# Performance work log

Hardware: AMD Instinct MI355X
Metric: run time of the kernel (lower is better)

## Reference

```python
import jax, jax.numpy as jnp
import numpy as np

D_MODEL = 1024
NUM_HEADS = 16
HEAD_DIM = D_MODEL // NUM_HEADS  # 64
N = 1024
B = 8


def setup_inputs() -> dict:
    key = jax.random.key(0)
    ks = jax.random.split(key, 11)
    s = 0.02
    inp = {
        'query': jax.random.normal(ks[0], (B, D_MODEL, N), jnp.float32),
        'key':   jax.random.normal(ks[1], (B, D_MODEL, N), jnp.float32),
        'value': jax.random.normal(ks[2], (B, D_MODEL, N), jnp.float32),
        # 1x1 conv1d == linear over channel dim: weight [out, in], bias [out]
        'Wq': jax.random.normal(ks[3], (D_MODEL, D_MODEL), jnp.float32) * s,
        'bq': jax.random.normal(ks[4], (D_MODEL,), jnp.float32) * s,
        'Wk': jax.random.normal(ks[5], (D_MODEL, D_MODEL), jnp.float32) * s,
        'bk': jax.random.normal(ks[6], (D_MODEL,), jnp.float32) * s,
        'Wv': jax.random.normal(ks[7], (D_MODEL, D_MODEL), jnp.float32) * s,
        'bv': jax.random.normal(ks[8], (D_MODEL,), jnp.float32) * s,
        'Wm': jax.random.normal(ks[9], (D_MODEL, D_MODEL), jnp.float32) * s,
        'bm': jax.random.normal(ks[10], (D_MODEL,), jnp.float32) * s,
    }
    return inp


def _proj(W, b, x):
    # nn.Conv1d(kernel_size=1): out[b,o,n] = sum_i W[o,i] x[b,i,n] + b[o]
    return jnp.einsum('oi,bin->bon', W, x) + b[None, :, None]


def reference(query, key, value, Wq, bq, Wk, bk, Wv, bv, Wm, bm):
    Bd = query.shape[0]
    # view(B, dim, heads, N): channel axis split as (head_dim, num_heads)
    q = _proj(Wq, bq, query).reshape(Bd, HEAD_DIM, NUM_HEADS, -1)
    k = _proj(Wk, bk, key).reshape(Bd, HEAD_DIM, NUM_HEADS, -1)
    v = _proj(Wv, bv, value).reshape(Bd, HEAD_DIM, NUM_HEADS, -1)
    scale = 1.0 / (HEAD_DIM ** 0.5)
    scores = jnp.einsum('bdhn,bdhm->bhnm', q, k) * scale  # [B,H,N,N]
    prob = jax.nn.softmax(scores, axis=-1)
    x = jnp.einsum('bhnm,bdhm->bdhn', prob, v)  # [B,D,H,N]
    out = _proj(Wm, bm, x.reshape(Bd, HEAD_DIM * NUM_HEADS, -1))
    return out
```

## Files before the change

kernel.cpp:

```cpp
#include <hip/hip_runtime.h>

typedef __bf16 bf16x8 __attribute__((ext_vector_type(8)));
typedef __bf16 bf16x4 __attribute__((ext_vector_type(4)));
typedef float f32x4 __attribute__((ext_vector_type(4)));
typedef unsigned short u16;
typedef unsigned int u32;

typedef union { bf16x8 v8; bf16x4 v4[2]; } bfu;

__device__ __forceinline__ u16 f2bf(float f) {
  u32 u = __builtin_bit_cast(u32, f);
  u = (u + 0x7FFFu + ((u >> 16) & 1u)) >> 16;
  return (u16)u;
}

__device__ __forceinline__ void gload_lds16(const void* g, void* l) {
  __builtin_amdgcn_global_load_lds((const __attribute__((address_space(1))) void*)g,
                                   (__attribute__((address_space(3))) void*)l, 16, 0, 0);
}

__global__ __launch_bounds__(256) void transpose_cast3(const float* __restrict__ q,
                                                       const float* __restrict__ k,
                                                       const float* __restrict__ v,
                                                       u16* __restrict__ X3) {
  __shared__ float T[64][68];
  int tid = threadIdx.x;
  int n0 = blockIdx.x * 64, i0 = blockIdx.y * 64;
  int z = blockIdx.z;
  int which = z >> 3, b = z & 7;
  const float* src = (which == 0) ? q : (which == 1) ? k : v;
  size_t boff = (size_t)b << 20;
  const float* s = src + boff;
  u16* d = X3 + ((size_t)which << 23) + boff;
  int ir = tid >> 4, n4 = (tid & 15) * 4;
#pragma unroll
  for (int r = 0; r < 4; ++r) {
    int i_loc = ir + r * 16;
    float4 vv = *(const float4*)(s + (size_t)(i0 + i_loc) * 1024 + n0 + n4);
    *(float4*)&T[i_loc][n4] = vv;
  }
  __syncthreads();
  int nr = tid >> 3, i8 = (tid & 7) * 8;
#pragma unroll
  for (int r = 0; r < 2; ++r) {
    int n_loc = nr + r * 32;
    u32 pk[4];
#pragma unroll
    for (int j = 0; j < 4; ++j) {
      float f0 = T[i8 + 2 * j][n_loc];
      float f1 = T[i8 + 2 * j + 1][n_loc];
      pk[j] = (u32)f2bf(f0) | ((u32)f2bf(f1) << 16);
    }
    *(uint4*)(d + (size_t)(n0 + n_loc) * 1024 + i0 + i8) = make_uint4(pk[0], pk[1], pk[2], pk[3]);
  }
}

__global__ __launch_bounds__(256) void transpose_cast(const float* __restrict__ src,
                                                      u16* __restrict__ dst) {
  __shared__ float T[64][68];
  int tid = threadIdx.x;
  int n0 = blockIdx.x * 64, i0 = blockIdx.y * 64;
  size_t boff = (size_t)blockIdx.z << 20;
  const float* s = src + boff;
  u16* d = dst + boff;
  int ir = tid >> 4, n4 = (tid & 15) * 4;
#pragma unroll
  for (int r = 0; r < 4; ++r) {
    int i_loc = ir + r * 16;
    float4 v = *(const float4*)(s + (size_t)(i0 + i_loc) * 1024 + n0 + n4);
    *(float4*)&T[i_loc][n4] = v;
  }
  __syncthreads();
  int nr = tid >> 3, i8 = (tid & 7) * 8;
#pragma unroll
  for (int r = 0; r < 2; ++r) {
    int n_loc = nr + r * 32;
    u32 pk[4];
#pragma unroll
    for (int j = 0; j < 4; ++j) {
      float f0 = T[i8 + 2 * j][n_loc];
      float f1 = T[i8 + 2 * j + 1][n_loc];
      pk[j] = (u32)f2bf(f0) | ((u32)f2bf(f1) << 16);
    }
    *(uint4*)(d + (size_t)(n0 + n_loc) * 1024 + i0 + i8) = make_uint4(pk[0], pk[1], pk[2], pk[3]);
  }
}

__global__ __launch_bounds__(256) void cast_weights(const float* __restrict__ Wq,
                                                    const float* __restrict__ Wk,
                                                    const float* __restrict__ Wv,
                                                    const float* __restrict__ Wm,
                                                    u16* __restrict__ out) {
  int w = blockIdx.y;
  const float* src = (w == 0) ? Wq : (w == 1) ? Wk : (w == 2) ? Wv : Wm;
  u16* dst = out + ((size_t)w << 20);
  int o = blockIdx.x;
  int c4 = threadIdx.x * 4;
  float f[4];
  if (w < 3) {
    float4 v = *(const float4*)(src + (size_t)o * 1024 + c4);
    f[0] = v.x; f[1] = v.y; f[2] = v.z; f[3] = v.w;
  } else {
#pragma unroll
    for (int j = 0; j < 4; ++j) {
      int cp = c4 + j;
      f[j] = src[(size_t)o * 1024 + (cp & 63) * 16 + (cp >> 6)];
    }
  }
  u32 p0 = (u32)f2bf(f[0]) | ((u32)f2bf(f[1]) << 16);
  u32 p1 = (u32)f2bf(f[2]) | ((u32)f2bf(f[3]) << 16);
  *(uint2*)(dst + (size_t)o * 1024 + c4) = make_uint2(p0, p1);
}

__device__ __forceinline__ void gemm_body(const u16* __restrict__ A,
                                          const u16* __restrict__ B,
                                          const float* __restrict__ bias,
                                          void* __restrict__ Out, float escale,
                                          int epi, u16* LD) {
  int tid = threadIdx.x;
  int wave = tid >> 6, l = tid & 63, ln = l & 15, g = l >> 4;
  int wm = wave >> 1, wn = wave & 1;
  int bid = blockIdx.x;
  int mt = (bid >> 3) & 7;
  int nt = ((bid & 7) << 2) | (bid >> 6);
  int c0 = mt * 128, n0 = nt * 256;

  int R = tid >> 3;
  int v = (tid & 7) ^ (R & 7);
  const u16* aS = A + (size_t)(c0 + 2 * R + (v >> 2)) * 1024 + (v & 3) * 8;
  const u16* bS = B + (size_t)(n0 + 2 * R + (v >> 2)) * 1024 + (v & 3) * 8;

  int slr = ((((ln & 1) << 2) | g) ^ ((ln >> 1) & 7)) * 8;
  int laneA = (wm * 32 + (ln >> 1)) * 64 + slr;
  int laneB = (wn * 64 + (ln >> 1)) * 64 + slr;

  f32x4 acc[4][8] = {};

#define STAGE(buf, kt)                                                        \
  do {                                                                        \
    gload_lds16(aS + (kt) * 32, &LD[(buf) * 4096 + tid * 8]);                 \
    gload_lds16(aS + 65536 + (kt) * 32, &LD[(buf) * 4096 + 2048 + tid * 8]);  \
    gload_lds16(bS + (kt) * 32, &LD[12288 + (buf) * 8192 + tid * 8]);         \
    gload_lds16(bS + 65536 + (kt) * 32,                                       \
                &LD[12288 + (buf) * 8192 + 2048 + tid * 8]);                  \
    gload_lds16(bS + 131072 + (kt) * 32,                                      \
                &LD[12288 + (buf) * 8192 + 4096 + tid * 8]);                  \
    gload_lds16(bS + 196608 + (kt) * 32,                                      \
                &LD[12288 + (buf) * 8192 + 6144 + tid * 8]);                  \
  } while (0)

  STAGE(0, 0);
  STAGE(1, 1);

#pragma unroll
  for (int t = 0; t < 32; ++t) {
    if (t < 31)
      asm volatile("s_waitcnt vmcnt(6)" ::: "memory");
    else
      asm volatile("s_waitcnt vmcnt(0)" ::: "memory");
    asm volatile("s_barrier" ::: "memory");
    if (t <= 29) STAGE((t + 2) % 3, t + 2);
    const int ab = (t % 3) * 4096;
    const int bb = 12288 + (t % 3) * 8192;
    bf16x8 af[4];
#pragma unroll
    for (int mm = 0; mm < 4; ++mm) af[mm] = *(const bf16x8*)&LD[ab + laneA + mm * 512];
    __builtin_amdgcn_s_setprio(1);
#pragma unroll
    for (int nn = 0; nn < 8; ++nn) {
      bf16x8 bfr = *(const bf16x8*)&LD[bb + laneB + nn * 512];
#pragma unroll
      for (int mm = 0; mm < 4; ++mm)
        acc[mm][nn] = __builtin_amdgcn_mfma_f32_16x16x32_bf16(af[mm], bfr, acc[mm][nn], 0, 0, 0);
    }
    __builtin_amdgcn_s_setprio(0);
  }
#undef STAGE

  int D0 = (c0 >> 4) + wm * 4;
#pragma unroll
  for (int nn = 0; nn < 8; ++nn) {
    size_t ng = (size_t)n0 + wn * 128 + nn * 16 + ln;
#pragma unroll
    for (int r = 0; r < 4; ++r) {
      int h = g * 4 + r;
      if (epi == 0) {
        bf16x4 pk;
#pragma unroll
        for (int mm = 0; mm < 4; ++mm) {
          int c = c0 + wm * 64 + mm * 16 + h;
          pk[mm] = (__bf16)((acc[mm][nn][r] + bias[c]) * escale);
        }
        *(bf16x4*)((u16*)Out + ng * 1024 + (size_t)h * 64 + D0) = pk;
      } else {
        size_t b = ng >> 10, n = ng & 1023;
#pragma unroll
        for (int mm = 0; mm < 4; ++mm) {
          int c = c0 + wm * 64 + mm * 16 + h;
          float val = (acc[mm][nn][r] + bias[c]) * escale;
          if (epi == 1) {
            int d = D0 + mm;
            ((u16*)Out)[((b * 16 + h) * 64 + d) * 1024 + n] = f2bf(val);
          } else {
            ((float*)Out)[(b << 20) + (size_t)c * 1024 + n] = val;
          }
        }
      }
    }
  }
}

template <int EPI>
__global__ __launch_bounds__(256, 2) void gemm4b(const u16* __restrict__ A,
                                                 const u16* __restrict__ B,
                                                 const float* __restrict__ bias,
                                                 void* __restrict__ Out, float escale) {
  __shared__ u16 LD[36864];
  gemm_body(A, B, bias, Out, escale, EPI, LD);
}

__global__ __launch_bounds__(256, 2) void gemm_qkv(const u16* __restrict__ Wbf,
                                                   const u16* __restrict__ X3,
                                                   const float* __restrict__ bq,
                                                   const float* __restrict__ bk,
                                                   const float* __restrict__ bv,
                                                   u16* __restrict__ Qh,
                                                   u16* __restrict__ Kh,
                                                   u16* __restrict__ Vt, float qscale) {
  __shared__ u16 LD[36864];
  int z = blockIdx.y;
  const u16* A = Wbf + ((size_t)z << 20);
  const u16* B = X3 + ((size_t)z << 23);
  const float* bias = (z == 0) ? bq : (z == 1) ? bk : bv;
  void* Out = (z == 0) ? (void*)Qh : (z == 1) ? (void*)Kh : (void*)Vt;
  float escale = (z == 0) ? qscale : 1.0f;
  int epi = (z == 2) ? 1 : 0;
  gemm_body(A, B, bias, Out, escale, epi, LD);
}

__global__ __launch_bounds__(256, 2) void attn_kernel(const u16* __restrict__ Qh,
                                                      const u16* __restrict__ Kh,
                                                      const u16* __restrict__ Vt,
                                                      u16* __restrict__ Xh) {
  __shared__ u16 Ks[2][4096];
  __shared__ u16 Vs[2][4096];
  int tid = threadIdx.x;
  int w = tid >> 6, l = tid & 63, ln = l & 15, g = l >> 4;
  int id = blockIdx.x;
  int bh7 = id & 7;
  int qp = (id >> 3) & 3;
  int bh = (id >> 5) * 8 + bh7;
  size_t b = bh >> 4;
  int h = bh & 15;
  const u16* Qg = Qh + (b << 20) + (h << 6);
  const u16* Kg = Kh + (b << 20) + (h << 6);
  const u16* Vg = Vt + ((size_t)bh << 16);
  u16* Og = Xh + (b << 20) + (h << 6);

  bf16x8 qf[4][2];
#pragma unroll
  for (int t = 0; t < 4; ++t)
#pragma unroll
    for (int kk = 0; kk < 2; ++kk)
      qf[t][kk] = *(const bf16x8*)(Qg + (size_t)(qp * 256 + t * 64 + w * 16 + ln) * 1024 + kk * 32 + g * 8);

  int lr = l >> 3;
  int sw8 = ((l & 7) ^ lr) << 3;
  int r0 = w * 16 + lr, r1 = r0 + 8;
  const u16* kS0 = Kg + (size_t)r0 * 1024 + sw8;
  const u16* kS1 = Kg + (size_t)r1 * 1024 + sw8;
  const u16* vS0 = Vg + (size_t)r0 * 1024 + sw8;
  const u16* vS1 = Vg + (size_t)r1 * 1024 + sw8;

  f32x4 xacc[4][4] = {};
  float lacc[4] = {0.f, 0.f, 0.f, 0.f};

  gload_lds16(kS0, &Ks[0][(w * 2) * 512]);
  gload_lds16(kS1, &Ks[0][(w * 2 + 1) * 512]);
  gload_lds16(vS0, &Vs[0][(w * 2) * 512]);
  gload_lds16(vS1, &Vs[0][(w * 2 + 1) * 512]);
  __syncthreads();

  int sx = ln & 7;
  int cur = 0;
  for (int kt = 0; kt < 16; ++kt) {
    if (kt < 15) {
      int nxt = cur ^ 1;
      gload_lds16(kS0 + (size_t)(kt + 1) * 65536, &Ks[nxt][(w * 2) * 512]);
      gload_lds16(kS1 + (size_t)(kt + 1) * 65536, &Ks[nxt][(w * 2 + 1) * 512]);
      gload_lds16(vS0 + (kt + 1) * 64, &Vs[nxt][(w * 2) * 512]);
      gload_lds16(vS1 + (kt + 1) * 64, &Vs[nxt][(w * 2 + 1) * 512]);
    }
    bf16x8 kf[2][4];
#pragma unroll
    for (int kk = 0; kk < 2; ++kk)
#pragma unroll
      for (int f = 0; f < 4; ++f) {
        int slot = (((kk << 2) + g) ^ sx) << 3;
        kf[kk][f] = *(const bf16x8*)&Ks[cur][(f * 16 + ln) * 64 + slot];
      }
    bf16x8 vf[2][4];
#pragma unroll
    for (int kk = 0; kk < 2; ++kk) {
      int s0 = (kk << 2) + (g >> 1);
      int off = (g & 1) << 2;
#pragma unroll
      for (int fd = 0; fd < 4; ++fd) {
        int rowb = (fd * 16 + ln) * 64;
        bfu uv;
        uv.v4[0] = *(const bf16x4*)&Vs[cur][rowb + ((s0 ^ sx) << 3) + off];
        uv.v4[1] = *(const bf16x4*)&Vs[cur][rowb + (((s0 + 2) ^ sx) << 3) + off];
        vf[kk][fd] = uv.v8;
      }
    }
#pragma unroll
    for (int t = 0; t < 4; ++t) {
      f32x4 sacc[4] = {};
#pragma unroll
      for (int kk = 0; kk < 2; ++kk)
#pragma unroll
        for (int f = 0; f < 4; ++f)
          sacc[f] = __builtin_amdgcn_mfma_f32_16x16x32_bf16(kf[kk][f], qf[t][kk], sacc[f], 0, 0, 0);
      bf16x8 pf[2];
#pragma unroll
      for (int kk = 0; kk < 2; ++kk) {
        bfu up;
#pragma unroll
        for (int e2 = 0; e2 < 2; ++e2) {
          int f = 2 * kk + e2;
          float p0 = __builtin_amdgcn_exp2f(sacc[f][0]);
          float p1 = __builtin_amdgcn_exp2f(sacc[f][1]);
          float p2 = __builtin_amdgcn_exp2f(sacc[f][2]);
          float p3 = __builtin_amdgcn_exp2f(sacc[f][3]);
          lacc[t] += (p0 + p1) + (p2 + p3);
          bf16x4 pb;
          pb[0] = (__bf16)p0; pb[1] = (__bf16)p1; pb[2] = (__bf16)p2; pb[3] = (__bf16)p3;
          up.v4[e2] = pb;
        }
        pf[kk] = up.v8;
      }
#pragma unroll
      for (int kk = 0; kk < 2; ++kk)
#pragma unroll
        for (int fd = 0; fd < 4; ++fd)
          xacc[t][fd] = __builtin_amdgcn_mfma_f32_16x16x32_bf16(pf[kk], vf[kk][fd], xacc[t][fd], 0, 0, 0);
    }
    __syncthreads();
    cur ^= 1;
  }

#pragma unroll
  for (int t = 0; t < 4; ++t) {
    float lt = lacc[t];
    lt += __shfl_xor(lt, 16);
    lt += __shfl_xor(lt, 32);
    float il[4];
#pragma unroll
    for (int r = 0; r < 4; ++r) il[r] = 1.0f / __shfl(lt, g * 4 + r);
#pragma unroll
    for (int fd = 0; fd < 4; ++fd)
#pragma unroll
      for (int r = 0; r < 4; ++r) {
        int nq = qp * 256 + t * 64 + w * 16 + g * 4 + r;
        Og[(size_t)nq * 1024 + fd * 16 + ln] = f2bf(xacc[t][fd][r] * il[r]);
      }
  }
}

extern "C" void kernel_launch(void* const* d_in, const int* in_sizes, int n_in,
                              void* d_out, int out_size, void* d_ws, size_t ws_size,
                              hipStream_t stream) {
  const float* q  = (const float*)d_in[0];
  const float* k  = (const float*)d_in[1];
  const float* v  = (const float*)d_in[2];
  const float* Wq = (const float*)d_in[3];
  const float* bq = (const float*)d_in[4];
  const float* Wk = (const float*)d_in[5];
  const float* bk = (const float*)d_in[6];
  const float* Wv = (const float*)d_in[7];
  const float* bv = (const float*)d_in[8];
  const float* Wm = (const float*)d_in[9];
  const float* bm = (const float*)d_in[10];

  char* ws = (char*)d_ws;
  u16* Wbf = (u16*)ws;
  u16* Qh  = (u16*)(ws + (8ull << 20));
  u16* Kh  = (u16*)(ws + (24ull << 20));
  u16* Vt  = (u16*)(ws + (40ull << 20));
  u16* X3  = (u16*)(ws + (56ull << 20));

  cast_weights<<<dim3(1024, 4, 1), 256, 0, stream>>>(Wq, Wk, Wv, Wm, Wbf);

  const float qscale = 0.125f * 1.44269504088896340736f;

  if (ws_size >= (104ull << 20)) {
    transpose_cast3<<<dim3(16, 16, 24), 256, 0, stream>>>(q, k, v, X3);
    gemm_qkv<<<dim3(256, 3), 256, 0, stream>>>(Wbf, X3, bq, bk, bv, Qh, Kh, Vt, qscale);
  } else {
    dim3 tg(16, 16, 8);
    transpose_cast<<<tg, 256, 0, stream>>>(q, X3);
    gemm4b<0><<<256, 256, 0, stream>>>(Wbf, X3, bq, Qh, qscale);
    transpose_cast<<<tg, 256, 0, stream>>>(k, X3);
    gemm4b<0><<<256, 256, 0, stream>>>(Wbf + (1u << 20), X3, bk, Kh, 1.0f);
    transpose_cast<<<tg, 256, 0, stream>>>(v, X3);
    gemm4b<1><<<256, 256, 0, stream>>>(Wbf + (2u << 20), X3, bv, Vt, 1.0f);
  }

  attn_kernel<<<512, 256, 0, stream>>>(Qh, Kh, Vt, X3);

  gemm4b<2><<<256, 256, 0, stream>>>(Wbf + (3u << 20), X3, bm, d_out, 1.0f);
}
```

Before: 171.9 us.

## Rewrite QKV projection GEMM with 256x256 tiles and 8-wave blocks

Replaces the shared gemm_body call in the fused QKV projection with a dedicated kernel that uses 512 threads (8 waves in a 2x4 grid) and 256x256 output tiles. It double-buffers K-slices in 128 KB of LDS using direct global-to-LDS loads and interleaves prefetches with MFMA groups under raised scheduling priority. The intent is more operand reuse per LDS load and better latency hiding. The cost is higher register and LDS pressure and only 384 blocks, which may leave compute units unevenly loaded.

```diff
diff --git a/kernel.cpp b/kernel.cpp
--- a/kernel.cpp
+++ b/kernel.cpp
@@ -219,15 +219,15 @@
   gemm_body(A, B, bias, Out, escale, EPI, LD);
 }
 
-__global__ __launch_bounds__(256, 2) void gemm_qkv(const u16* __restrict__ Wbf,
-                                                   const u16* __restrict__ X3,
-                                                   const float* __restrict__ bq,
-                                                   const float* __restrict__ bk,
-                                                   const float* __restrict__ bv,
-                                                   u16* __restrict__ Qh,
-                                                   u16* __restrict__ Kh,
-                                                   u16* __restrict__ Vt, float qscale) {
-  __shared__ u16 LD[36864];
+__global__ __launch_bounds__(512, 2) void gemm_qkv8(const u16* __restrict__ Wbf,
+                                                    const u16* __restrict__ X3,
+                                                    const float* __restrict__ bq,
+                                                    const float* __restrict__ bk,
+                                                    const float* __restrict__ bv,
+                                                    u16* __restrict__ Qh,
+                                                    u16* __restrict__ Kh,
+                                                    u16* __restrict__ Vt, float qscale) {
+  __shared__ u16 LD[65536];
   int z = blockIdx.y;
   const u16* A = Wbf + ((size_t)z << 20);
   const u16* B = X3 + ((size_t)z << 23);
@@ -235,7 +235,126 @@
   void* Out = (z == 0) ? (void*)Qh : (z == 1) ? (void*)Kh : (void*)Vt;
   float escale = (z == 0) ? qscale : 1.0f;
   int epi = (z == 2) ? 1 : 0;
-  gemm_body(A, B, bias, Out, escale, epi, LD);
+
+  int tid = threadIdx.x;
+  int wave = tid >> 6, l = tid & 63, ln = l & 15, g = l >> 4;
+  int wm = wave >> 2, wn = wave & 3;
+  int bid = blockIdx.x;
+  int work = (bid & 7) * 16 + (bid >> 3);
+  int mt = work >> 5, nt = work & 31;
+  int c0 = mt * 256, n0 = nt * 256;
+
+  int r0 = tid >> 2;
+  int sw = ((tid & 3) ^ ((tid >> 3) & 3)) * 8;
+  const u16* aS = A + (size_t)(c0 + r0) * 1024 + sw;
+  const u16* bS = B + (size_t)(n0 + r0) * 1024 + sw;
+  int dst0 = tid * 8;
+
+  int swr = (g ^ ((ln >> 1) & 3)) * 8;
+  int laneA = (wm * 128 + ln) * 32 + swr;
+  int laneB = 32768 + (wn * 64 + ln) * 32 + swr;
+
+  f32x4 acc[8][4] = {};
+
+#define SU(op, kkv, kt, buf)                                              \
+  do {                                                                    \
+    const u16* s_ = ((op) ? bS : aS) + (kt) * 64 + (kkv) * 32;            \
+    int d_ = ((op) ? 32768 : 0) + (buf) * 16384 + (kkv) * 8192 + dst0;    \
+    gload_lds16(s_, &LD[d_]);                                             \
+    gload_lds16(s_ + 131072, &LD[d_ + 4096]);                             \
+  } while (0)
+
+  SU(0, 0, 0, 0);
+  SU(1, 0, 0, 0);
+  SU(0, 1, 0, 0);
+  SU(1, 1, 0, 0);
+
+#pragma unroll
+  for (int kt = 0; kt < 16; ++kt) {
+    const int buf = kt & 1;
+    const int abase = buf * 16384;
+    bf16x8 af[4], bf0[4];
+    asm volatile("s_waitcnt vmcnt(4)" ::: "memory");
+    asm volatile("s_barrier" ::: "memory");
+#pragma unroll
+    for (int m = 0; m < 4; ++m) af[m] = *(const bf16x8*)&LD[abase + laneA + m * 512];
+#pragma unroll
+    for (int nn = 0; nn < 4; ++nn) bf0[nn] = *(const bf16x8*)&LD[abase + laneB + nn * 512];
+    if (kt < 15) SU(0, 0, kt + 1, buf ^ 1);
+    __builtin_amdgcn_s_setprio(1);
+#pragma unroll
+    for (int m = 0; m < 4; ++m)
+#pragma unroll
+      for (int nn = 0; nn < 4; ++nn)
+        acc[m][nn] = __builtin_amdgcn_mfma_f32_16x16x32_bf16(af[m], bf0[nn], acc[m][nn], 0, 0, 0);
+    __builtin_amdgcn_s_setprio(0);
+#pragma unroll
+    for (int m = 0; m < 4; ++m) af[m] = *(const bf16x8*)&LD[abase + laneA + (m + 4) * 512];
+    if (kt < 15) SU(1, 0, kt + 1, buf ^ 1);
+    __builtin_amdgcn_s_setprio(1);
+#pragma unroll
+    for (int m = 0; m < 4; ++m)
+#pragma unroll
+      for (int nn = 0; nn < 4; ++nn)
+        acc[m + 4][nn] = __builtin_amdgcn_mfma_f32_16x16x32_bf16(af[m], bf0[nn], acc[m + 4][nn], 0, 0, 0);
+    __builtin_amdgcn_s_setprio(0);
+    if (kt < 15)
+      asm volatile("s_waitcnt vmcnt(4)" ::: "memory");
+    else
+      asm volatile("s_waitcnt vmcnt(0)" ::: "memory");
+    asm volatile("s_barrier" ::: "memory");
+#pragma unroll
+    for (int m = 0; m < 4; ++m) af[m] = *(const bf16x8*)&LD[abase + 8192 + laneA + m * 512];
+#pragma unroll
+    for (int nn = 0; nn < 4; ++nn) bf0[nn] = *(const bf16x8*)&LD[abase + 8192 + laneB + nn * 512];
+    if (kt < 15) SU(0, 1, kt + 1, buf ^ 1);
+    __builtin_amdgcn_s_setprio(1);
+#pragma unroll
+    for (int m = 0; m < 4; ++m)
+#pragma unroll
+      for (int nn = 0; nn < 4; ++nn)
+        acc[m][nn] = __builtin_amdgcn_mfma_f32_16x16x32_bf16(af[m], bf0[nn], acc[m][nn], 0, 0, 0);
+    __builtin_amdgcn_s_setprio(0);
+#pragma unroll
+    for (int m = 0; m < 4; ++m) af[m] = *(const bf16x8*)&LD[abase + 8192 + laneA + (m + 4) * 512];
+    if (kt < 15) SU(1, 1, kt + 1, buf ^ 1);
+    __builtin_amdgcn_s_setprio(1);
+#pragma unroll
+    for (int m = 0; m < 4; ++m)
+#pragma unroll
+      for (int nn = 0; nn < 4; ++nn)
+        acc[m + 4][nn] = __builtin_amdgcn_mfma_f32_16x16x32_bf16(af[m], bf0[nn], acc[m + 4][nn], 0, 0, 0);
+    __builtin_amdgcn_s_setprio(0);
+  }
+#undef SU
+
+  int D0 = (c0 >> 4) + wm * 8;
+#pragma unroll
+  for (int nn = 0; nn < 4; ++nn) {
+    size_t ng = (size_t)n0 + wn * 64 + nn * 16 + ln;
+#pragma unroll
+    for (int r = 0; r < 4; ++r) {
+      int h = g * 4 + r;
+      if (epi == 0) {
+        bf16x8 pk;
+#pragma unroll
+        for (int m = 0; m < 8; ++m) {
+          int c = c0 + wm * 128 + m * 16 + h;
+          pk[m] = (__bf16)((acc[m][nn][r] + bias[c]) * escale);
+        }
+        *(bf16x8*)((u16*)Out + ng * 1024 + (size_t)h * 64 + D0) = pk;
+      } else {
+        size_t b = ng >> 10, n = ng & 1023;
+#pragma unroll
+        for (int m = 0; m < 8; ++m) {
+          int c = c0 + wm * 128 + m * 16 + h;
+          float val = (acc[m][nn][r] + bias[c]) * escale;
+          int d = D0 + m;
+          ((u16*)Out)[((b * 16 + h) * 64 + d) * 1024 + n] = f2bf(val);
+        }
+      }
+    }
+  }
 }
 
 __global__ __launch_bounds__(256, 2) void attn_kernel(const u16* __restrict__ Qh,
@@ -395,7 +514,7 @@
 
   if (ws_size >= (104ull << 20)) {
     transpose_cast3<<<dim3(16, 16, 24), 256, 0, stream>>>(q, k, v, X3);
-    gemm_qkv<<<dim3(256, 3), 256, 0, stream>>>(Wbf, X3, bq, bk, bv, Qh, Kh, Vt, qscale);
+    gemm_qkv8<<<dim3(128, 3), 512, 0, stream>>>(Wbf, X3, bq, bk, bv, Qh, Kh, Vt, qscale);
   } else {
     dim3 tg(16, 16, 8);
     transpose_cast<<<tg, 256, 0, stream>>>(q, X3);
```

New measurement: 182.8 us. 6.3% more time.
